# Kernel optimization log

Hardware: AMD Instinct MI355X
Metric: run time of the kernel (lower is better)

## Reference

```python
import jax, jax.numpy as jnp
import numpy as np

B, S, D, H, HD, E, DE = 2, 512, 768, 12, 64, 50, 50  # batch, seq, input_dim, heads, head_dim, edge_dim, dep_embed_dim


def setup_inputs() -> dict:
    key = jax.random.key(0)
    ks = jax.random.split(key, 16)
    def xn(k, shape, s=0.02):
        return (jax.random.normal(k, shape, jnp.float32) * s)
    return {
        'weight_prob_softmax': jax.random.uniform(ks[0], (B, S, S, E), jnp.float32),
        'weight_adj': jax.random.normal(ks[1], (B, S, S, E), jnp.float32),
        'gcn_inputs': jax.random.normal(ks[2], (B, S, D), jnp.float32),
        'self_loop': jax.random.uniform(ks[3], (B, S, S, E), jnp.float32),
        # self.linear
        'W_lin': xn(ks[4], (D, D)), 'b_lin': jnp.zeros((D,), jnp.float32),
        # additive attention vectors fc_w1 / fc_w2 (stored [H, HD])
        'fc_w1': xn(ks[5], (H, HD), 0.2), 'fc_w2': xn(ks[6], (H, HD), 0.2),
        # edge_mlp: Linear(E,128) -> ReLU -> (Dropout eval) -> Linear(128,H)
        'We1': xn(ks[7], (128, E), 0.1), 'be1': jnp.zeros((128,), jnp.float32),
        'We2': xn(ks[8], (H, 128), 0.1), 'be2': jnp.zeros((H,), jnp.float32),
        # self.W output projection
        'W_out': xn(ks[9], (D, D)), 'b_out': jnp.zeros((D,), jnp.float32),
        # LayerNorm params
        'ln_a': jnp.ones((D,), jnp.float32), 'ln_b': jnp.zeros((D,), jnp.float32),
        # highway.W split into column blocks: [edge | edge_i | edge_j | node1 | node2]
        'Wh_e': xn(ks[10], (DE, E), 0.1), 'Wh_ei': xn(ks[11], (DE, E), 0.1),
        'Wh_ej': xn(ks[12], (DE, E), 0.1), 'Wh_n1': xn(ks[13], (DE, D), 0.05),
        'Wh_n2': xn(ks[14], (DE, D), 0.05), 'bh': jnp.zeros((DE,), jnp.float32),
    }


def reference(weight_prob_softmax, weight_adj, gcn_inputs, self_loop,
              W_lin, b_lin, fc_w1, fc_w2, We1, be1, We2, be2,
              W_out, b_out, ln_a, ln_b, Wh_e, Wh_ei, Wh_ej, Wh_n1, Wh_n2, bh):
    wps = self_loop + weight_prob_softmax                      # [B,S,S,E]
    mask = jnp.sum(wps, axis=-1) == 0.0                        # [B,S,S]
    feature = (gcn_inputs @ W_lin.T + b_lin).reshape(B, S, H, HD)
    attn_src = jnp.einsum('bshd,hd->bhs', feature, fc_w1)      # [B,H,S]
    attn_dst = jnp.einsum('bshd,hd->bhs', feature, fc_w2)      # [B,H,S]
    # edge MLP bias (dropout is identity in eval)
    hmid = jax.nn.relu(jnp.einsum('bije,fe->bijf', wps, We1) + be1)  # [B,S,S,128]
    A = jnp.einsum('bijf,hf->bhij', hmid, We2) + be2[None, :, None, None]  # [B,H,S,S]
    attn = jax.nn.leaky_relu(attn_src[:, :, :, None] + attn_dst[:, :, None, :] + A,
                             negative_slope=0.01)
    attn = jnp.where(mask[:, None, :, :], -jnp.inf, attn)
    attn = jax.nn.softmax(attn, axis=-1)
    gcn = jnp.einsum('bhij,bjhd->bihd', attn, feature).reshape(B, S, D)
    gcn = gcn @ W_out.T + b_out
    # torch LayerNorm variant: unbiased std, divide by (std + eps)
    mean = jnp.mean(gcn, axis=-1, keepdims=True)
    std = jnp.std(gcn, axis=-1, ddof=1, keepdims=True)
    gcn = ln_a * (gcn - mean) / (std + 1e-6) + ln_b
    node = jax.nn.relu(gcn)                                    # [B,S,D]
    # RefiningStrategy: W([edge, edge_i, edge_j, node1, node2]) via block matmuls
    ediag = jnp.diagonal(weight_adj, axis1=1, axis2=2).transpose(0, 2, 1)  # [B,S,E]
    edge_out = (jnp.einsum('bije,fe->bijf', weight_adj, Wh_e)
                + (ediag @ Wh_ei.T)[:, :, None, :]             # edge_i[b,i,j]=diag[b,i]
                + (ediag @ Wh_ej.T)[:, None, :, :]             # edge_j[b,i,j]=diag[b,j]
                + (node @ Wh_n1.T)[:, None, :, :]              # node1[b,i,j]=node[b,j]
                + (node @ Wh_n2.T)[:, :, None, :]              # node2[b,i,j]=node[b,i]
                + bh)                                          # [B,S,S,DE]
    return node, edge_out
```

## Files before the change

### kernel.cpp

```cpp
#include <hip/hip_runtime.h>
#include <math.h>
#include <stddef.h>

#define BB 2
#define SS 512
#define DD 768
#define HH 12
#define HDIM 64
#define EE 50
#define DE 50
#define F1 128

typedef float f32x4 __attribute__((ext_vector_type(4)));
typedef short s16x8 __attribute__((ext_vector_type(8)));

static __device__ __forceinline__ unsigned short f2bf(float x) {
  unsigned int u = __float_as_uint(x);
  unsigned int r = u + 0x7fffu + ((u >> 16) & 1u);
  return (unsigned short)(r >> 16);
}
static __device__ __forceinline__ float bf2f(unsigned short b) {
  return __uint_as_float(((unsigned int)b) << 16);
}

__global__ __launch_bounds__(256) void k_gemm_bias(
    const float* __restrict__ X, int ldx,
    const float* __restrict__ W,
    const float* __restrict__ bias,
    float* __restrict__ Y, int ldy,
    int M, int N, int K)
{
  __shared__ float Xs[32][68];
  __shared__ float Ws[32][68];
  int t = threadIdx.x;
  int tx = t & 15, ty = t >> 4;
  int m0 = blockIdx.y * 64, n0 = blockIdx.x * 64;
  float acc[4][4] = {};
  for (int k0 = 0; k0 < K; k0 += 32) {
#pragma unroll
    for (int q = 0; q < 2; ++q) {
      int idx = t + q * 256;
      int r = idx >> 3, c = (idx & 7) << 2;
      float4 v = *(const float4*)(X + (size_t)(m0 + r) * ldx + k0 + c);
      Xs[c + 0][r] = v.x; Xs[c + 1][r] = v.y; Xs[c + 2][r] = v.z; Xs[c + 3][r] = v.w;
      float4 w = *(const float4*)(W + (size_t)(n0 + r) * K + k0 + c);
      Ws[c + 0][r] = w.x; Ws[c + 1][r] = w.y; Ws[c + 2][r] = w.z; Ws[c + 3][r] = w.w;
    }
    __syncthreads();
#pragma unroll
    for (int kk = 0; kk < 32; ++kk) {
      float a[4], b[4];
#pragma unroll
      for (int u = 0; u < 4; ++u) a[u] = Xs[kk][ty * 4 + u];
#pragma unroll
      for (int u = 0; u < 4; ++u) b[u] = Ws[kk][tx * 4 + u];
#pragma unroll
      for (int i = 0; i < 4; ++i)
#pragma unroll
        for (int j = 0; j < 4; ++j) acc[i][j] += a[i] * b[j];
    }
    __syncthreads();
  }
#pragma unroll
  for (int i = 0; i < 4; ++i) {
    int m = m0 + ty * 4 + i;
#pragma unroll
    for (int j = 0; j < 4; ++j) {
      int n = n0 + tx * 4 + j;
      Y[(size_t)m * ldy + n] = acc[i][j] + bias[n];
    }
  }
}

__global__ __launch_bounds__(192) void k_attnvec(
    const float* __restrict__ feat, const float* __restrict__ w1,
    const float* __restrict__ w2, float* __restrict__ src, float* __restrict__ dst)
{
  int bs = blockIdx.x;
  int t = threadIdx.x;
  int h = t >> 4, l = t & 15;
  float4 f = *(const float4*)(feat + (size_t)bs * DD + h * HDIM + l * 4);
  float4 a = *(const float4*)(w1 + h * HDIM + l * 4);
  float4 c = *(const float4*)(w2 + h * HDIM + l * 4);
  float ps = f.x * a.x + f.y * a.y + f.z * a.z + f.w * a.w;
  float pd = f.x * c.x + f.y * c.y + f.z * c.z + f.w * c.w;
#pragma unroll
  for (int o = 8; o > 0; o >>= 1) {
    ps += __shfl_xor(ps, o);
    pd += __shfl_xor(pd, o);
  }
  if (l == 0) {
    int b = bs >> 9, s = bs & 511;
    src[((b * HH + h) << 9) + s] = ps;
    dst[((b * HH + h) << 9) + s] = pd;
  }
}

__global__ __launch_bounds__(64) void k_prep(
    const float* __restrict__ We1, const float* __restrict__ be1,
    const float* __restrict__ We2, const float* __restrict__ Whe,
    s16x8* __restrict__ wtab, float* __restrict__ betab,
    s16x8* __restrict__ wtabE)
{
  const int l = threadIdx.x;
  const int lr = l & 15, lg = l >> 4;
#pragma unroll
  for (int ks = 0; ks < 2; ++ks)
#pragma unroll
    for (int n = 0; n < 8; ++n) {
      s16x8 v;
#pragma unroll
      for (int u = 0; u < 8; ++u) {
        int e = ks * 32 + lg * 8 + u;
        float x = (e < 50) ? We1[(n * 16 + lr) * 50 + e] : 0.0f;
        v[u] = (short)f2bf(x);
      }
      wtab[(ks * 8 + n) * 64 + l] = v;
    }
#pragma unroll
  for (int kk = 0; kk < 4; ++kk) {
    s16x8 v;
#pragma unroll
    for (int u = 0; u < 8; ++u) {
      int f = kk * 32 + lg * 8 + u;
      v[u] = (short)((lr < 12) ? f2bf(We2[lr * 128 + f]) : (unsigned short)0);
    }
    wtab[(16 + kk) * 64 + l] = v;
  }
#pragma unroll
  for (int n = 0; n < 8; ++n) betab[n * 64 + l] = be1[n * 16 + lr];
#pragma unroll
  for (int nt = 0; nt < 4; ++nt)
#pragma unroll
    for (int ks = 0; ks < 2; ++ks) {
      int f = nt * 16 + lr;
      s16x8 v;
#pragma unroll
      for (int u = 0; u < 8; ++u) {
        int e = ks * 32 + lg * 8 + u;
        float x = (f < 50 && e < 50) ? Whe[f * 50 + e] : 0.0f;
        v[u] = (short)f2bf(x);
      }
      wtabE[(nt * 2 + ks) * 64 + l] = v;
    }
}

__global__ __launch_bounds__(256, 3) void k_scores_mfma(
    const float* __restrict__ wprob, const float* __restrict__ sloop,
    const s16x8* __restrict__ wtab, const float* __restrict__ betab,
    const float* __restrict__ be2,
    const float* __restrict__ src, const float* __restrict__ dst,
    float* __restrict__ scores)
{
  __shared__ unsigned short wps_s[128][72];
  __shared__ unsigned short hmid_s[128][132];
  __shared__ float masks[128];

  const int blk = blockIdx.x;
  const int c = blk & 3;
  const int i = (blk >> 2) & 511;
  const int b = blk >> 11;
  const int j0c = c << 7;
  const int t = threadIdx.x;
  const int w = t >> 6, l = t & 63;
  const int lr = l & 15, lg = l >> 4;
  const int jbase = w * 32;

  const size_t rowbase = (size_t)(b * SS + i) * SS * EE + (size_t)c * 6400;
  float4 pw[7], psl[7];
  {
    const float* wp = wprob + rowbase;
    const float* sl = sloop + rowbase;
#pragma unroll
    for (int k = 0; k < 7; ++k)
      if (k < 6 || t < 64) {
        pw[k] = *(const float4*)(wp + 4 * (t + 256 * k));
        psl[k] = *(const float4*)(sl + 4 * (t + 256 * k));
      }
  }

  s16x8 wa[2][8];
#pragma unroll
  for (int ks = 0; ks < 2; ++ks)
#pragma unroll
    for (int n = 0; n < 8; ++n) wa[ks][n] = wtab[(ks * 8 + n) * 64 + l];
  s16x8 wb[4];
#pragma unroll
  for (int kk = 0; kk < 4; ++kk) wb[kk] = wtab[(16 + kk) * 64 + l];
  float be1v[8];
#pragma unroll
  for (int n = 0; n < 8; ++n) be1v[n] = betab[n * 64 + l];
  const int hc = (lr < 12) ? lr : 0;
  const float be2v = be2[hc];
  const float srcv = src[((b * HH + hc) << 9) + i];
  const float* drow = dst + ((size_t)(b * HH + hc) << 9);
  float4 dv0 = *(const float4*)(drow + j0c + jbase + lg * 4);
  float4 dv1 = *(const float4*)(drow + j0c + jbase + 16 + lg * 4);

  for (int q = t; q < 896; q += 256) {
    int r = q / 7, cd = 25 + q % 7;
    ((unsigned int*)wps_s)[r * 36 + cd] = 0u;
  }

#pragma unroll
  for (int k = 0; k < 7; ++k)
    if (k < 6 || t < 64) {
      int f = 4 * (t + 256 * k);
      int j = f / 50;
      int e0 = f - j * 50;
      float vs[4] = {pw[k].x + psl[k].x, pw[k].y + psl[k].y,
                     pw[k].z + psl[k].z, pw[k].w + psl[k].w};
#pragma unroll
      for (int u = 0; u < 4; ++u) {
        int e = e0 + u, jj = j;
        if (e >= 50) { e -= 50; jj += 1; }
        wps_s[jj][e] = f2bf(vs[u]);
      }
    }
  __syncthreads();

  if (l < 32) {
    const unsigned short* row = wps_s[jbase + l];
    float s = 0.0f;
#pragma unroll
    for (int q = 0; q < 6; ++q) {
      s16x8 v = *(const s16x8*)(row + q * 8);
#pragma unroll
      for (int u = 0; u < 8; ++u) s += bf2f((unsigned short)v[u]);
    }
    unsigned int last = *(const unsigned int*)(row + 48);
    s += bf2f((unsigned short)(last & 0xffffu)) + bf2f((unsigned short)(last >> 16));
    masks[jbase + l] = (s == 0.0f) ? 1.0f : 0.0f;
  }

  f32x4 accA[2][8] = {};
#pragma unroll
  for (int ks = 0; ks < 2; ++ks) {
    s16x8 a0 = *(const s16x8*)&wps_s[jbase + lr][ks * 32 + lg * 8];
    s16x8 a1 = *(const s16x8*)&wps_s[jbase + 16 + lr][ks * 32 + lg * 8];
#pragma unroll
    for (int n = 0; n < 8; ++n) {
      accA[0][n] = __builtin_amdgcn_mfma_f32_16x16x32_bf16(a0, wa[ks][n], accA[0][n], 0, 0, 0);
      accA[1][n] = __builtin_amdgcn_mfma_f32_16x16x32_bf16(a1, wa[ks][n], accA[1][n], 0, 0, 0);
    }
  }
#pragma unroll
  for (int jt = 0; jt < 2; ++jt)
#pragma unroll
    for (int n = 0; n < 8; ++n)
#pragma unroll
      for (int r = 0; r < 4; ++r) {
        float v = fmaxf(accA[jt][n][r] + be1v[n], 0.0f);
        hmid_s[jbase + jt * 16 + lg * 4 + r][n * 16 + lr] = f2bf(v);
      }

  f32x4 accB[2] = {};
#pragma unroll
  for (int kk = 0; kk < 4; ++kk) {
    s16x8 a0 = *(const s16x8*)&hmid_s[jbase + lr][kk * 32 + lg * 8];
    s16x8 a1 = *(const s16x8*)&hmid_s[jbase + 16 + lr][kk * 32 + lg * 8];
    accB[0] = __builtin_amdgcn_mfma_f32_16x16x32_bf16(a0, wb[kk], accB[0], 0, 0, 0);
    accB[1] = __builtin_amdgcn_mfma_f32_16x16x32_bf16(a1, wb[kk], accB[1], 0, 0, 0);
  }

  if (lr < 12) {
#pragma unroll
    for (int jt = 0; jt < 2; ++jt) {
      int jl = jbase + jt * 16 + lg * 4;
      const float4 dv = jt ? dv1 : dv0;
      float4 st;
#pragma unroll
      for (int r = 0; r < 4; ++r) {
        float x = accB[jt][r] + be2v + srcv + (&dv.x)[r];
        x = (x > 0.0f) ? x : 0.01f * x;
        if (masks[jl + r] != 0.0f) x = -INFINITY;
        (&st.x)[r] = x;
      }
      *(float4*)(scores + ((((size_t)(b * SS + i)) * HH + lr) << 9) + j0c + jl) = st;
    }
  }
}

__global__ __launch_bounds__(256) void k_softmax_pv(
    const float* __restrict__ scores, const float* __restrict__ feat,
    float* __restrict__ gout)
{
  __shared__ float p[2][12][512];
  int blk = blockIdx.x;
  int b = blk >> 8;
  int i0 = (blk & 255) << 1;
  int t = threadIdx.x;
  size_t base = ((size_t)(b * SS + i0) * HH) << 9;
  for (int q = t; q < 12288; q += 256) ((float*)p)[q] = scores[base + q];
  __syncthreads();

  int w = t >> 6, l = t & 63;
  for (int r = w; r < 24; r += 4) {
    int ii = r / 12, h = r % 12;
    float* row = p[ii][h];
    float vv[8];
    float m = -INFINITY;
#pragma unroll
    for (int u = 0; u < 8; ++u) {
      vv[u] = row[l + (u << 6)];
      m = fmaxf(m, vv[u]);
    }
#pragma unroll
    for (int o = 32; o > 0; o >>= 1) m = fmaxf(m, __shfl_xor(m, o));
    float s = 0.0f;
#pragma unroll
    for (int u = 0; u < 8; ++u) {
      float e = __expf(vv[u] - m);
      vv[u] = e;
      s += e;
    }
#pragma unroll
    for (int o = 32; o > 0; o >>= 1) s += __shfl_xor(s, o);
    float inv = 1.0f / s;
#pragma unroll
    for (int u = 0; u < 8; ++u) row[l + (u << 6)] = vv[u] * inv;
  }
  __syncthreads();

  float acc[2][3] = {};
  const float* fb = feat + (size_t)b * SS * DD;
  int h0 = t >> 6;
#pragma unroll 4
  for (int j = 0; j < 512; ++j) {
    const float* fr = fb + (size_t)j * DD;
    float f0 = fr[t], f1 = fr[t + 256], f2 = fr[t + 512];
    float p00 = p[0][h0][j], p10 = p[1][h0][j];
    float p01 = p[0][h0 + 4][j], p11 = p[1][h0 + 4][j];
    float p02 = p[0][h0 + 8][j], p12 = p[1][h0 + 8][j];
    acc[0][0] += p00 * f0; acc[0][1] += p01 * f1; acc[0][2] += p02 * f2;
    acc[1][0] += p10 * f0; acc[1][1] += p11 * f1; acc[1][2] += p12 * f2;
  }
#pragma unroll
  for (int ii = 0; ii < 2; ++ii)
#pragma unroll
    for (int u = 0; u < 3; ++u)
      gout[(size_t)(b * SS + i0 + ii) * DD + t + (u << 8)] = acc[ii][u];
}

__global__ __launch_bounds__(256) void k_ln(
    const float* __restrict__ gcn2, const float* __restrict__ ga,
    const float* __restrict__ gb, float* __restrict__ out)
{
  __shared__ float rs[4], rss[4];
  int row = blockIdx.x;
  int t = threadIdx.x;
  const float* x = gcn2 + (size_t)row * DD;
  float v[3];
  float s = 0.0f, ss2 = 0.0f;
#pragma unroll
  for (int u = 0; u < 3; ++u) {
    v[u] = x[t + (u << 8)];
    s += v[u];
    ss2 += v[u] * v[u];
  }
#pragma unroll
  for (int o = 32; o > 0; o >>= 1) {
    s += __shfl_down(s, o);
    ss2 += __shfl_down(ss2, o);
  }
  int w = t >> 6, l = t & 63;
  if (l == 0) { rs[w] = s; rss[w] = ss2; }
  __syncthreads();
  float S = rs[0] + rs[1] + rs[2] + rs[3];
  float SSum = rss[0] + rss[1] + rss[2] + rss[3];
  float mean = S * (1.0f / 768.0f);
  float var = (SSum - 768.0f * mean * mean) * (1.0f / 767.0f);
  var = fmaxf(var, 0.0f);
  float rinv = 1.0f / (sqrtf(var) + 1e-6f);
#pragma unroll
  for (int u = 0; u < 3; ++u) {
    int cidx = t + (u << 8);
    float y = ga[cidx] * (v[u] - mean) * rinv + gb[cidx];
    out[(size_t)row * DD + cidx] = fmaxf(y, 0.0f);
  }
}

__global__ __launch_bounds__(256) void k_pq(
    const float* __restrict__ node, const float* __restrict__ wadj,
    const float* __restrict__ Whei, const float* __restrict__ Whej,
    const float* __restrict__ Whn1, const float* __restrict__ Whn2,
    const float* __restrict__ bh, float* __restrict__ P, float* __restrict__ Q)
{
  __shared__ float nd[2][768];
  __shared__ float ed[2][64];
  const int bs0 = blockIdx.x * 2;
  const int t = threadIdx.x;
  const int w = t >> 6, l = t & 63;

  for (int q = t; q < 384; q += 256) {
    int rr = q / 192, idx = q % 192;
    *(float4*)(nd[rr] + idx * 4) =
        *(const float4*)(node + (size_t)(bs0 + rr) * DD + idx * 4);
  }
  {
    int rr = t >> 7, tt = t & 127;
    if (tt < 50) {
      int bs = bs0 + rr;
      int b = bs >> 9, s = bs & 511;
      ed[rr][tt] = wadj[((size_t)(b * SS + s) * SS + s) * EE + tt];
    }
  }
  __syncthreads();

  float4 n00 = *(const float4*)(nd[0] + l * 4);
  float4 n01 = *(const float4*)(nd[0] + 256 + l * 4);
  float4 n02 = *(const float4*)(nd[0] + 512 + l * 4);
  float4 n10 = *(const float4*)(nd[1] + l * 4);
  float4 n11 = *(const float4*)(nd[1] + 256 + l * 4);
  float4 n12 = *(const float4*)(nd[1] + 512 + l * 4);
  float el0 = (l < 50) ? ed[0][l] : 0.0f;
  float el1 = (l < 50) ? ed[1][l] : 0.0f;

  for (int o = w; o < 100; o += 4) {
    const int which = (o >= 50);
    const int f = o - which * 50;
    const float* Wn = which ? Whn1 : Whn2;
    const float* We = which ? Whej : Whei;
    const float* wr = Wn + f * DD;
    float4 w0 = *(const float4*)(wr + l * 4);
    float4 w1 = *(const float4*)(wr + 256 + l * 4);
    float4 w2 = *(const float4*)(wr + 512 + l * 4);
    float wev = (l < 50) ? We[f * EE + l] : 0.0f;
    float a0 = n00.x * w0.x + n00.y * w0.y + n00.z * w0.z + n00.w * w0.w
             + n01.x * w1.x + n01.y * w1.y + n01.z * w1.z + n01.w * w1.w
             + n02.x * w2.x + n02.y * w2.y + n02.z * w2.z + n02.w * w2.w
             + el0 * wev;
    float a1 = n10.x * w0.x + n10.y * w0.y + n10.z * w0.z + n10.w * w0.w
             + n11.x * w1.x + n11.y * w1.y + n11.z * w1.z + n11.w * w1.w
             + n12.x * w2.x + n12.y * w2.y + n12.z * w2.z + n12.w * w2.w
             + el1 * wev;
#pragma unroll
    for (int ofs = 32; ofs > 0; ofs >>= 1) {
      a0 += __shfl_xor(a0, ofs);
      a1 += __shfl_xor(a1, ofs);
    }
    if (l == 0) {
      float bias = which ? bh[f] : 0.0f;
      float* dst0 = (which ? Q : P) + (size_t)bs0 * DE + f;
      dst0[0] = a0 + bias;
      dst0[DE] = a1 + bias;
    }
  }
}

__global__ __launch_bounds__(256) void k_edge_mfma(
    const float* __restrict__ wadj, const s16x8* __restrict__ wtabE,
    const float* __restrict__ P, const float* __restrict__ Q,
    float* __restrict__ eout)
{
  __shared__ unsigned short adj_s[128][72];
  __shared__ float P_s[64];

  const int t = threadIdx.x;
  const size_t n0 = (size_t)blockIdx.x * 128;
  const int b = (int)(n0 >> 18);
  const int i = (int)((n0 & 262143) >> 9);
  const int j0 = (int)(n0 & 511);
  const int w = t >> 6, l = t & 63;
  const int lr = l & 15, lg = l >> 4;
  const int mbase = w * 32;

  float4 pw[7];
  {
    const float* wp = wadj + n0 * EE;
#pragma unroll
    for (int k = 0; k < 7; ++k)
      if (k < 6 || t < 64) pw[k] = *(const float4*)(wp + 4 * (t + 256 * k));
  }

  s16x8 we[4][2];
#pragma unroll
  for (int nt = 0; nt < 4; ++nt)
#pragma unroll
    for (int ks = 0; ks < 2; ++ks) we[nt][ks] = wtabE[(nt * 2 + ks) * 64 + l];
  if (t < 64) P_s[t] = (t < 50) ? P[(size_t)(b * SS + i) * DE + t] : 0.0f;

  for (int q = t; q < 896; q += 256) {
    int r = q / 7, cd = 25 + q % 7;
    ((unsigned int*)adj_s)[r * 36 + cd] = 0u;
  }

#pragma unroll
  for (int k = 0; k < 7; ++k)
    if (k < 6 || t < 64) {
      int f = 4 * (t + 256 * k);
      int j = f / 50;
      int e0 = f - j * 50;
#pragma unroll
      for (int u = 0; u < 4; ++u) {
        int e = e0 + u, jj = j;
        if (e >= 50) { e -= 50; jj += 1; }
        adj_s[jj][e] = f2bf((&pw[k].x)[u]);
      }
    }
  __syncthreads();

  f32x4 acc[2][4] = {};
#pragma unroll
  for (int ks = 0; ks < 2; ++ks) {
    s16x8 a0 = *(const s16x8*)&adj_s[mbase + lr][ks * 32 + lg * 8];
    s16x8 a1 = *(const s16x8*)&adj_s[mbase + 16 + lr][ks * 32 + lg * 8];
#pragma unroll
    for (int nt = 0; nt < 4; ++nt) {
      acc[0][nt] = __builtin_amdgcn_mfma_f32_16x16x32_bf16(a0, we[nt][ks], acc[0][nt], 0, 0, 0);
      acc[1][nt] = __builtin_amdgcn_mfma_f32_16x16x32_bf16(a1, we[nt][ks], acc[1][nt], 0, 0, 0);
    }
  }

#pragma unroll
  for (int nt = 0; nt < 4; ++nt) {
    int f = nt * 16 + lr;
    if (f < 50) {
      float pf = P_s[f];
#pragma unroll
      for (int mt = 0; mt < 2; ++mt) {
        int m = mbase + mt * 16 + lg * 4;
        const float* qp = Q + (size_t)(b * SS + j0 + m) * DE + f;
        float* op = eout + (n0 + m) * DE + f;
#pragma unroll
        for (int r = 0; r < 4; ++r)
          op[r * DE] = acc[mt][nt][r] + pf + qp[r * DE];
      }
    }
  }
}

extern "C" void kernel_launch(void* const* d_in, const int* in_sizes, int n_in,
                              void* d_out, int out_size, void* d_ws, size_t ws_size,
                              hipStream_t stream)
{
  const float* wprob = (const float*)d_in[0];
  const float* wadj  = (const float*)d_in[1];
  const float* gin   = (const float*)d_in[2];
  const float* sloop = (const float*)d_in[3];
  const float* W_lin = (const float*)d_in[4];
  const float* b_lin = (const float*)d_in[5];
  const float* fw1   = (const float*)d_in[6];
  const float* fw2   = (const float*)d_in[7];
  const float* We1   = (const float*)d_in[8];
  const float* be1   = (const float*)d_in[9];
  const float* We2   = (const float*)d_in[10];
  const float* be2   = (const float*)d_in[11];
  const float* W_out = (const float*)d_in[12];
  const float* b_out = (const float*)d_in[13];
  const float* ln_a  = (const float*)d_in[14];
  const float* ln_b  = (const float*)d_in[15];
  const float* Whe   = (const float*)d_in[16];
  const float* Whei  = (const float*)d_in[17];
  const float* Whej  = (const float*)d_in[18];
  const float* Whn1  = (const float*)d_in[19];
  const float* Whn2  = (const float*)d_in[20];
  const float* bh    = (const float*)d_in[21];

  float* ws = (float*)d_ws;
  float* feature = ws + 0;
  float* src     = ws + 786432;
  float* dst     = ws + 798720;
  float* scores  = ws + 811008;
  float* gcnmid  = ws + 7102464;
  float* gcn2    = ws + 7888896;
  float* P       = ws + 8675328;
  float* Q       = ws + 8726528;
  s16x8* wtab    = (s16x8*)(ws + 8777728);
  float* betab   = ws + 8782848;
  s16x8* wtabE   = (s16x8*)(ws + 8783360);

  float* node = (float*)d_out;
  float* eout = (float*)d_out + 786432;

  k_prep<<<1, 64, 0, stream>>>(We1, be1, We2, Whe, wtab, betab, wtabE);
  k_gemm_bias<<<dim3(DD / 64, (BB * SS) / 64), 256, 0, stream>>>(
      gin, DD, W_lin, b_lin, feature, DD, BB * SS, DD, DD);
  k_attnvec<<<BB * SS, 192, 0, stream>>>(feature, fw1, fw2, src, dst);
  k_scores_mfma<<<BB * SS * 4, 256, 0, stream>>>(
      wprob, sloop, wtab, betab, be2, src, dst, scores);
  k_softmax_pv<<<BB * SS / 2, 256, 0, stream>>>(scores, feature, gcnmid);
  k_gemm_bias<<<dim3(DD / 64, (BB * SS) / 64), 256, 0, stream>>>(
      gcnmid, DD, W_out, b_out, gcn2, DD, BB * SS, DD, DD);
  k_ln<<<BB * SS, 256, 0, stream>>>(gcn2, ln_a, ln_b, node);
  k_pq<<<BB * SS / 2, 256, 0, stream>>>(node, wadj, Whei, Whej, Whn1, Whn2, bh, P, Q);
  k_edge_mfma<<<(BB * SS * SS) / 128, 256, 0, stream>>>(wadj, wtabE, P, Q, eout);
}
```

Baseline: 302.2 us.

## Split edge-MLP hidden layer into halves and stage edge output through LDS

The scores kernel now computes the 128-wide hidden layer in two 64-column halves, loading only half of the first-layer weight fragments at a time and feeding each half straight into the second MFMA. This shrinks the hmid LDS buffer and the register footprint, and the launch bound is raised from 3 to 4 blocks per CU to use that for occupancy. The edge kernel writes its tile into a shared staging buffer and then stores it to global memory as contiguous float4 writes, replacing strided scalar stores. This costs an extra barrier and more LDS per block.

Result: faster. 284.2 us (-5.9%).

```diff
diff --git a/kernel.cpp b/kernel.cpp
--- a/kernel.cpp
+++ b/kernel.cpp
@@ -145,7 +145,7 @@
     }
 }
 
-__global__ __launch_bounds__(256, 3) void k_scores_mfma(
+__global__ __launch_bounds__(256, 4) void k_scores_mfma(
     const float* __restrict__ wprob, const float* __restrict__ sloop,
     const s16x8* __restrict__ wtab, const float* __restrict__ betab,
     const float* __restrict__ be2,
@@ -153,7 +153,7 @@
     float* __restrict__ scores)
 {
   __shared__ unsigned short wps_s[128][72];
-  __shared__ unsigned short hmid_s[128][132];
+  __shared__ unsigned short hmid_s[128][72];
   __shared__ float masks[128];
 
   const int blk = blockIdx.x;
@@ -179,11 +179,6 @@
       }
   }
 
-  s16x8 wa[2][8];
-#pragma unroll
-  for (int ks = 0; ks < 2; ++ks)
-#pragma unroll
-    for (int n = 0; n < 8; ++n) wa[ks][n] = wtab[(ks * 8 + n) * 64 + l];
   s16x8 wb[4];
 #pragma unroll
   for (int kk = 0; kk < 4; ++kk) wb[kk] = wtab[(16 + kk) * 64 + l];
@@ -233,34 +228,49 @@
     masks[jbase + l] = (s == 0.0f) ? 1.0f : 0.0f;
   }
 
-  f32x4 accA[2][8] = {};
+  s16x8 aA[2][2];
 #pragma unroll
   for (int ks = 0; ks < 2; ++ks) {
-    s16x8 a0 = *(const s16x8*)&wps_s[jbase + lr][ks * 32 + lg * 8];
-    s16x8 a1 = *(const s16x8*)&wps_s[jbase + 16 + lr][ks * 32 + lg * 8];
-#pragma unroll
-    for (int n = 0; n < 8; ++n) {
-      accA[0][n] = __builtin_amdgcn_mfma_f32_16x16x32_bf16(a0, wa[ks][n], accA[0][n], 0, 0, 0);
-      accA[1][n] = __builtin_amdgcn_mfma_f32_16x16x32_bf16(a1, wa[ks][n], accA[1][n], 0, 0, 0);
-    }
-  }
-#pragma unroll
-  for (int jt = 0; jt < 2; ++jt)
-#pragma unroll
-    for (int n = 0; n < 8; ++n)
-#pragma unroll
-      for (int r = 0; r < 4; ++r) {
-        float v = fmaxf(accA[jt][n][r] + be1v[n], 0.0f);
-        hmid_s[jbase + jt * 16 + lg * 4 + r][n * 16 + lr] = f2bf(v);
-      }
+    aA[0][ks] = *(const s16x8*)&wps_s[jbase + lr][ks * 32 + lg * 8];
+    aA[1][ks] = *(const s16x8*)&wps_s[jbase + 16 + lr][ks * 32 + lg * 8];
+  }
 
   f32x4 accB[2] = {};
 #pragma unroll
-  for (int kk = 0; kk < 4; ++kk) {
-    s16x8 a0 = *(const s16x8*)&hmid_s[jbase + lr][kk * 32 + lg * 8];
-    s16x8 a1 = *(const s16x8*)&hmid_s[jbase + 16 + lr][kk * 32 + lg * 8];
-    accB[0] = __builtin_amdgcn_mfma_f32_16x16x32_bf16(a0, wb[kk], accB[0], 0, 0, 0);
-    accB[1] = __builtin_amdgcn_mfma_f32_16x16x32_bf16(a1, wb[kk], accB[1], 0, 0, 0);
+  for (int h = 0; h < 2; ++h) {
+    s16x8 wah[2][4];
+#pragma unroll
+    for (int ks = 0; ks < 2; ++ks)
+#pragma unroll
+      for (int nn = 0; nn < 4; ++nn)
+        wah[ks][nn] = wtab[(ks * 8 + h * 4 + nn) * 64 + l];
+
+    f32x4 accA[2][4] = {};
+#pragma unroll
+    for (int ks = 0; ks < 2; ++ks)
+#pragma unroll
+      for (int nn = 0; nn < 4; ++nn) {
+        accA[0][nn] = __builtin_amdgcn_mfma_f32_16x16x32_bf16(aA[0][ks], wah[ks][nn], accA[0][nn], 0, 0, 0);
+        accA[1][nn] = __builtin_amdgcn_mfma_f32_16x16x32_bf16(aA[1][ks], wah[ks][nn], accA[1][nn], 0, 0, 0);
+      }
+#pragma unroll
+    for (int jt = 0; jt < 2; ++jt)
+#pragma unroll
+      for (int nn = 0; nn < 4; ++nn)
+#pragma unroll
+        for (int r = 0; r < 4; ++r) {
+          float v = fmaxf(accA[jt][nn][r] + be1v[h * 4 + nn], 0.0f);
+          hmid_s[jbase + jt * 16 + lg * 4 + r][nn * 16 + lr] = f2bf(v);
+        }
+
+#pragma unroll
+    for (int kh = 0; kh < 2; ++kh) {
+      int kk = 2 * h + kh;
+      s16x8 a0 = *(const s16x8*)&hmid_s[jbase + lr][kh * 32 + lg * 8];
+      s16x8 a1 = *(const s16x8*)&hmid_s[jbase + 16 + lr][kh * 32 + lg * 8];
+      accB[0] = __builtin_amdgcn_mfma_f32_16x16x32_bf16(a0, wb[kk], accB[0], 0, 0, 0);
+      accB[1] = __builtin_amdgcn_mfma_f32_16x16x32_bf16(a1, wb[kk], accB[1], 0, 0, 0);
+    }
   }
 
   if (lr < 12) {
@@ -453,7 +463,9 @@
     const float* __restrict__ P, const float* __restrict__ Q,
     float* __restrict__ eout)
 {
-  __shared__ unsigned short adj_s[128][72];
+  __shared__ __align__(16) unsigned char raw[25600];
+  unsigned short (*adj_s)[72] = (unsigned short(*)[72])raw;
+  float* park = (float*)raw;
   __shared__ float P_s[64];
 
   const int t = threadIdx.x;
@@ -511,6 +523,7 @@
       acc[1][nt] = __builtin_amdgcn_mfma_f32_16x16x32_bf16(a1, we[nt][ks], acc[1][nt], 0, 0, 0);
     }
   }
+  __syncthreads();
 
 #pragma unroll
   for (int nt = 0; nt < 4; ++nt) {
@@ -521,13 +534,17 @@
       for (int mt = 0; mt < 2; ++mt) {
         int m = mbase + mt * 16 + lg * 4;
         const float* qp = Q + (size_t)(b * SS + j0 + m) * DE + f;
-        float* op = eout + (n0 + m) * DE + f;
 #pragma unroll
         for (int r = 0; r < 4; ++r)
-          op[r * DE] = acc[mt][nt][r] + pf + qp[r * DE];
-      }
-    }
-  }
+          park[(m + r) * DE + f] = acc[mt][nt][r] + pf + qp[r * DE];
+      }
+    }
+  }
+  __syncthreads();
+
+  const float4* s4 = (const float4*)park;
+  float4* d4 = (float4*)(eout + n0 * DE);
+  for (int q = t; q < 1600; q += 256) d4[q] = s4[q];
 }
 
 extern "C" void kernel_launch(void* const* d_in, const int* in_sizes, int n_in,
```
